# Kernel optimization log

Measured on AMD Instinct MI355X. Metric: run time of the kernel, lower is better.

Reference implementation:

```python
import jax, jax.numpy as jnp
import numpy as np

VOCAB = 1_000_000
EMBED = 128
N_DENSE = 13
N_SPARSE = 26
BATCH = 16384
BOT_DIMS = [512, 256, 128]
TOP_DIMS = [1024, 1024, 512, 256, 1]


def setup_inputs() -> dict:
    key = jax.random.key(0)
    ks = list(jax.random.split(key, 32))
    # input: 13 dense floats + 26 categorical ids (stored as floats, cast in fwd)
    dense = jax.random.normal(ks[0], (BATCH, N_DENSE), dtype=jnp.float32)
    cat = jax.random.randint(ks[1], (BATCH, N_SPARSE), 0, VOCAB).astype(jnp.float32)
    x = jnp.concatenate([dense, cat], axis=1)
    inp = {"x": x, "train": 0}
    # bottom MLP params
    fan_in = N_DENSE
    for i, d in enumerate(BOT_DIMS):
        s = (6.0 / (fan_in + d)) ** 0.5  # glorot uniform scale
        inp[f"bw{i}"] = jax.random.uniform(ks[2 + 2 * i], (fan_in, d), jnp.float32, -s, s)
        inp[f"bb{i}"] = jax.random.normal(ks[3 + 2 * i], (d,), jnp.float32) * (1.0 / d) ** 0.5
        fan_in = d
    # unified embedding table
    inp["emb"] = jax.random.uniform(ks[10], (VOCAB, EMBED), jnp.float32) / jnp.sqrt(float(VOCAB))
    # top MLP params; input dim = embed_dim + triu(27) = 128 + 378 = 506
    n_feat = 1 + N_SPARSE  # bottom output contributes one 128-dim feature row
    fan_in = EMBED + (n_feat * (n_feat + 1)) // 2
    for i, d in enumerate(TOP_DIMS):
        std = (2.0 / (fan_in + d)) ** 0.5
        inp[f"tw{i}"] = jax.random.normal(ks[12 + 2 * i], (fan_in, d), jnp.float32) * std
        inp[f"tb{i}"] = jax.random.normal(ks[13 + 2 * i], (d,), jnp.float32) * (1.0 / d) ** 0.5
        fan_in = d
    return inp


def dot_interact(f):
    # f: [B, n, d]; keep_diags=True -> upper-triangular (incl. diag) of f @ f^T
    n = f.shape[1]
    iu, ju = jnp.triu_indices(n)
    xact = jnp.einsum('bnd,bmd->bnm', f, f)  # [B, n, n]
    return xact[:, iu, ju]  # [B, n*(n+1)/2]


def reference(x, train, bw0, bb0, bw1, bb1, bw2, bb2, emb,
              tw0, tb0, tw1, tb1, tw2, tb2, tw3, tb3, tw4, tb4):
    del train
    dense, cat = jnp.split(x, [N_DENSE], axis=1)
    idx = jnp.reshape(cat.astype(jnp.int32), [-1]) % VOCAB
    # bottom MLP
    h = dense
    for w, b in ((bw0, bb0), (bw1, bb1), (bw2, bb2)):
        h = jax.nn.relu(h @ w + b)
    bot_out = h  # [B, 128]
    B = bot_out.shape[0]
    feat = jnp.reshape(bot_out, [B, -1, EMBED])  # [B, 1, 128]
    embf = jnp.reshape(emb[idx], [B, -1, EMBED])  # [B, 26, 128]
    feat = jnp.concatenate([feat, embf], axis=1)  # [B, 27, 128]
    inter = dot_interact(feat)  # [B, 378]
    t = jnp.concatenate([bot_out, inter], axis=-1)  # [B, 506]
    tops = [(tw0, tb0), (tw1, tb1), (tw2, tb2), (tw3, tb3), (tw4, tb4)]
    for i, (w, b) in enumerate(tops):
        t = t @ w + b
        if i < len(tops) - 1:
            t = jax.nn.relu(t)
    return t  # [B, 1] logits
```

## Files before the change

kernel.cpp:

```cpp
#include <hip/hip_runtime.h>

typedef float v4f  __attribute__((ext_vector_type(4)));
typedef __bf16 bf16x8 __attribute__((ext_vector_type(8)));

__device__ __forceinline__ unsigned short f2bf(float f) {
    unsigned u = __builtin_bit_cast(unsigned, f);
    u += 0x7FFFu + ((u >> 16) & 1u);
    return (unsigned short)(u >> 16);
}
__device__ __forceinline__ float bf2f(unsigned short h) {
    return __builtin_bit_cast(float, (unsigned)h << 16);
}

__device__ __forceinline__ void gload16(const unsigned short* g, unsigned short* l) {
    __builtin_amdgcn_global_load_lds(
        (const __attribute__((address_space(1))) unsigned int*)g,
        (__attribute__((address_space(3))) unsigned int*)l, 16, 0, 0);
}

#define M_BATCH 16384

__global__ __launch_bounds__(256) void wprep(const float* __restrict__ in,
                                             unsigned short* __restrict__ out,
                                             int K, int N, int Kpad) {
    __shared__ float tile[32][33];
    int tx = threadIdx.x & 31;
    int ty = threadIdx.x >> 5;
    int n0 = blockIdx.x * 32, k0 = blockIdx.y * 32;
#pragma unroll
    for (int i = 0; i < 32; i += 8) {
        int k = k0 + ty + i, n = n0 + tx;
        tile[ty + i][tx] = (k < K && n < N) ? in[(size_t)k * N + n] : 0.f;
    }
    __syncthreads();
#pragma unroll
    for (int i = 0; i < 32; i += 8) {
        int n = n0 + ty + i, k = k0 + tx;
        if (n < N && k < Kpad) out[(size_t)n * Kpad + k] = f2bf(tile[tx][ty + i]);
    }
}

__global__ __launch_bounds__(256) void bot0(const float* __restrict__ x,
                                            const float* __restrict__ w,
                                            const float* __restrict__ b,
                                            unsigned short* __restrict__ h0) {
    int gid = blockIdx.x * 256 + threadIdx.x;
    int row = gid >> 9, col = gid & 511;
    const float* xr = x + (size_t)row * 39;
    float acc = b[col];
#pragma unroll
    for (int k = 0; k < 13; k++) acc += xr[k] * w[k * 512 + col];
    h0[gid] = f2bf(fmaxf(acc, 0.f));
}

__global__ __launch_bounds__(256) void gemm_bt(const unsigned short* __restrict__ A,
                                               const unsigned short* __restrict__ Bt,
                                               const float* __restrict__ bias,
                                               unsigned short* __restrict__ C,
                                               int N, int K, int relu) {
    __shared__ __align__(16) unsigned short As0[128 * 32];
    __shared__ __align__(16) unsigned short Bs0[128 * 32];
    __shared__ __align__(16) unsigned short As1[128 * 32];
    __shared__ __align__(16) unsigned short Bs1[128 * 32];
    const int tid  = threadIdx.x;
    const int wave = tid >> 6, lane = tid & 63;
    const int quad = lane >> 4, r16 = lane & 15;
    const int m_blk = blockIdx.y * 128, n_blk = blockIdx.x * 128;
    const int w_m = (wave >> 1) * 64, w_n = (wave & 1) * 64;

    v4f acc[4][4] = {};

    const int slot0 = tid, slot1 = tid + 256;
    const int rowS0 = slot0 >> 2, chS0 = slot0 & 3;
    const int rowS1 = slot1 >> 2, chS1 = slot1 & 3;

    const unsigned short* pa0 = A  + (size_t)(m_blk + rowS0) * K + chS0 * 8;
    const unsigned short* pa1 = A  + (size_t)(m_blk + rowS1) * K + chS1 * 8;
    const unsigned short* pb0 = Bt + (size_t)(n_blk + rowS0) * K + chS0 * 8;
    const unsigned short* pb1 = Bt + (size_t)(n_blk + rowS1) * K + chS1 * 8;

#define STAGE(AsX, BsX, kk)                                   \
    do {                                                      \
        gload16(pa0 + (kk), AsX + slot0 * 8);                 \
        gload16(pa1 + (kk), AsX + slot1 * 8);                 \
        gload16(pb0 + (kk), BsX + slot0 * 8);                 \
        gload16(pb1 + (kk), BsX + slot1 * 8);                 \
    } while (0)

#define DRAIN_BAR()                                           \
    do {                                                      \
        asm volatile("s_waitcnt vmcnt(0)" ::: "memory");      \
        __builtin_amdgcn_s_barrier();                         \
        __builtin_amdgcn_sched_barrier(0);                    \
    } while (0)

#define COMPUTE(AsX, BsX)                                                         \
    do {                                                                          \
        bf16x8 af[4], bf[4];                                                      \
        _Pragma("unroll")                                                         \
        for (int i = 0; i < 4; i++)                                               \
            af[i] = *(const bf16x8*)(AsX + (w_m + i * 16 + r16) * 32 + quad * 8); \
        _Pragma("unroll")                                                         \
        for (int j = 0; j < 4; j++)                                               \
            bf[j] = *(const bf16x8*)(BsX + (w_n + j * 16 + r16) * 32 + quad * 8); \
        _Pragma("unroll")                                                         \
        for (int i = 0; i < 4; i++)                                               \
            _Pragma("unroll")                                                     \
            for (int j = 0; j < 4; j++)                                           \
                acc[i][j] = __builtin_amdgcn_mfma_f32_16x16x32_bf16(              \
                    af[i], bf[j], acc[i][j], 0, 0, 0);                            \
    } while (0)

    STAGE(As0, Bs0, 0);
    DRAIN_BAR();

    for (int k0 = 0; k0 < K; k0 += 64) {
        STAGE(As1, Bs1, k0 + 32);
        COMPUTE(As0, Bs0);
        DRAIN_BAR();
        if (k0 + 64 < K) STAGE(As0, Bs0, k0 + 64);
        COMPUTE(As1, Bs1);
        DRAIN_BAR();
    }
#undef STAGE
#undef DRAIN_BAR
#undef COMPUTE

#pragma unroll
    for (int j = 0; j < 4; j++) {
        int gcol = n_blk + w_n + j * 16 + r16;
        float bv = bias[gcol];
#pragma unroll
        for (int i = 0; i < 4; i++) {
            int grow = m_blk + w_m + i * 16 + quad * 4;
#pragma unroll
            for (int r = 0; r < 4; r++) {
                float v = acc[i][j][r] + bv;
                if (relu) v = fmaxf(v, 0.f);
                C[(size_t)(grow + r) * N + gcol] = f2bf(v);
            }
        }
    }
}

#define FS 136
__global__ __launch_bounds__(256) void interact(const float* __restrict__ x,
                                                const float* __restrict__ emb,
                                                const unsigned short* __restrict__ h2,
                                                unsigned short* __restrict__ top_in) {
    __shared__ __align__(16) unsigned short feat[4][32 * FS];
    __shared__ __align__(16) unsigned short rowb[4][512];
    const int wave = threadIdx.x >> 6, lane = threadIdx.x & 63;
    const int s = blockIdx.x * 4 + wave;
    unsigned short* fw = feat[wave];
    unsigned short* rb = rowb[wave];
    const int quad = lane >> 4, r16 = lane & 15;

    int cat = 0;
    if (lane < 26) cat = (int)x[(size_t)s * 39 + 13 + lane];
    if (lane < 16)
        *(uint4*)(fw + lane * 8) = *(const uint4*)(h2 + (size_t)s * 128 + lane * 8);
#pragma unroll
    for (int i = 0; i < 13; i++) {
        int t = i * 64 + lane;
        int row = t >> 5, c4 = t & 31;
        int id = __shfl(cat, row);
        float4 v = *(const float4*)(emb + (size_t)id * 128 + c4 * 4);
        ushort4 o;
        o.x = f2bf(v.x); o.y = f2bf(v.y); o.z = f2bf(v.z); o.w = f2bf(v.w);
        *(ushort4*)(fw + (size_t)(row + 1) * FS + c4 * 4) = o;
    }
    v4f c00 = {0,0,0,0}, c01 = {0,0,0,0}, c11 = {0,0,0,0};
#pragma unroll
    for (int kc = 0; kc < 4; kc++) {
        bf16x8 a0 = *(const bf16x8*)(fw + r16 * FS + kc * 32 + quad * 8);
        bf16x8 a1 = *(const bf16x8*)(fw + (16 + r16) * FS + kc * 32 + quad * 8);
        c00 = __builtin_amdgcn_mfma_f32_16x16x32_bf16(a0, a0, c00, 0, 0, 0);
        c01 = __builtin_amdgcn_mfma_f32_16x16x32_bf16(a0, a1, c01, 0, 0, 0);
        c11 = __builtin_amdgcn_mfma_f32_16x16x32_bf16(a1, a1, c11, 0, 0, 0);
    }
    if (lane < 16) *(uint4*)(rb + lane * 8) = *(const uint4*)(fw + lane * 8);
    if (lane < 6) rb[506 + lane] = 0;
#pragma unroll
    for (int r = 0; r < 4; r++) {
        int i = quad * 4 + r;
        int j = r16;
        if (i <= j)
            rb[128 + i * 27 - (i * (i - 1)) / 2 + (j - i)] = f2bf(c00[r]);
        int j2 = 16 + r16;
        if (j2 < 27) {
            rb[128 + i * 27 - (i * (i - 1)) / 2 + (j2 - i)] = f2bf(c01[r]);
            int ii = 16 + quad * 4 + r;
            if (ii <= j2)
                rb[128 + ii * 27 - (ii * (ii - 1)) / 2 + (j2 - ii)] = f2bf(c11[r]);
        }
    }
    *(uint4*)(top_in + (size_t)s * 512 + lane * 8) = *(const uint4*)(rb + lane * 8);
}

__global__ __launch_bounds__(256) void top_final(const unsigned short* __restrict__ ht3,
                                                 const float* __restrict__ w,
                                                 const float* __restrict__ b,
                                                 float* __restrict__ out) {
    int wave = threadIdx.x >> 6, lane = threadIdx.x & 63;
    int row = blockIdx.x * 4 + wave;
    ushort4 av = *(const ushort4*)(ht3 + (size_t)row * 256 + lane * 4);
    float4 wv = *(const float4*)(w + lane * 4);
    float s = bf2f(av.x) * wv.x + bf2f(av.y) * wv.y + bf2f(av.z) * wv.z + bf2f(av.w) * wv.w;
#pragma unroll
    for (int off = 32; off; off >>= 1) s += __shfl_down(s, off);
    if (lane == 0) out[row] = s + b[0];
}

extern "C" void kernel_launch(void* const* d_in, const int* in_sizes, int n_in,
                              void* d_out, int out_size, void* d_ws, size_t ws_size,
                              hipStream_t stream) {
    (void)in_sizes; (void)n_in; (void)out_size; (void)ws_size;
    const float* x   = (const float*)d_in[0];
    const float* bw0 = (const float*)d_in[2];
    const float* bb0 = (const float*)d_in[3];
    const float* bw1 = (const float*)d_in[4];
    const float* bb1 = (const float*)d_in[5];
    const float* bw2 = (const float*)d_in[6];
    const float* bb2 = (const float*)d_in[7];
    const float* emb = (const float*)d_in[8];
    const float* tw0 = (const float*)d_in[9];
    const float* tb0 = (const float*)d_in[10];
    const float* tw1 = (const float*)d_in[11];
    const float* tb1 = (const float*)d_in[12];
    const float* tw2 = (const float*)d_in[13];
    const float* tb2 = (const float*)d_in[14];
    const float* tw3 = (const float*)d_in[15];
    const float* tb3 = (const float*)d_in[16];
    const float* tw4 = (const float*)d_in[17];
    const float* tb4 = (const float*)d_in[18];
    float* out = (float*)d_out;

    char* ws = (char*)d_ws;
    size_t off = 0;
    auto alloc = [&](size_t bytes) {
        void* p = ws + off;
        off += (bytes + 255) & ~(size_t)255;
        return p;
    };
    unsigned short* bw1t = (unsigned short*)alloc((size_t)256 * 512 * 2);
    unsigned short* bw2t = (unsigned short*)alloc((size_t)128 * 256 * 2);
    unsigned short* tw0t = (unsigned short*)alloc((size_t)1024 * 512 * 2);
    unsigned short* tw1t = (unsigned short*)alloc((size_t)1024 * 1024 * 2);
    unsigned short* tw2t = (unsigned short*)alloc((size_t)512 * 1024 * 2);
    unsigned short* tw3t = (unsigned short*)alloc((size_t)256 * 512 * 2);
    unsigned short* h2   = (unsigned short*)alloc((size_t)M_BATCH * 128 * 2);
    unsigned short* bufA = (unsigned short*)alloc((size_t)M_BATCH * 1024 * 2);
    unsigned short* bufB = (unsigned short*)alloc((size_t)M_BATCH * 1024 * 2);

    unsigned short* h0     = bufA;
    unsigned short* h1     = bufB;
    unsigned short* top_in = bufA;
    unsigned short* ht0    = bufB;
    unsigned short* ht1    = bufA;
    unsigned short* ht2    = bufB;
    unsigned short* ht3    = bufA;

    dim3 blk(256);
    wprep<<<dim3(256 / 32,  512 / 32),  blk, 0, stream>>>(bw1,  bw1t, 512,  256,  512);
    wprep<<<dim3(128 / 32,  256 / 32),  blk, 0, stream>>>(bw2,  bw2t, 256,  128,  256);
    wprep<<<dim3(1024 / 32, 512 / 32),  blk, 0, stream>>>(tw0,  tw0t, 506,  1024, 512);
    wprep<<<dim3(1024 / 32, 1024 / 32), blk, 0, stream>>>(tw1,  tw1t, 1024, 1024, 1024);
    wprep<<<dim3(512 / 32,  1024 / 32), blk, 0, stream>>>(tw2,  tw2t, 1024, 512,  1024);
    wprep<<<dim3(256 / 32,  512 / 32),  blk, 0, stream>>>(tw3,  tw3t, 512,  256,  512);

    bot0<<<dim3(M_BATCH * 512 / 256), blk, 0, stream>>>(x, bw0, bb0, h0);
    gemm_bt<<<dim3(256 / 128, M_BATCH / 128), blk, 0, stream>>>(h0, bw1t, bb1, h1, 256, 512, 1);
    gemm_bt<<<dim3(128 / 128, M_BATCH / 128), blk, 0, stream>>>(h1, bw2t, bb2, h2, 128, 256, 1);

    interact<<<dim3(M_BATCH / 4), blk, 0, stream>>>(x, emb, h2, top_in);

    gemm_bt<<<dim3(1024 / 128, M_BATCH / 128), blk, 0, stream>>>(top_in, tw0t, tb0, ht0, 1024, 512, 1);
    gemm_bt<<<dim3(1024 / 128, M_BATCH / 128), blk, 0, stream>>>(ht0, tw1t, tb1, ht1, 1024, 1024, 1);
    gemm_bt<<<dim3(512 / 128,  M_BATCH / 128), blk, 0, stream>>>(ht1, tw2t, tb2, ht2, 512, 1024, 1);
    gemm_bt<<<dim3(256 / 128,  M_BATCH / 128), blk, 0, stream>>>(ht2, tw3t, tb3, ht3, 256, 512, 1);
    top_final<<<dim3(M_BATCH / 4), blk, 0, stream>>>(ht3, tw4, tb4, out);
}
```

Measured before the change: 847.3 us.

## Replace direct-to-LDS loads with register-staged prefetch and remap workgroups across XCDs

The GEMM main loop stops using global_load_lds with a full vmcnt(0) drain. It now prefetches two K-tiles ahead into registers, waits only with vmcnt(4), and writes to LDS before an lgkmcnt barrier, so global loads overlap the MFMA compute. It also remaps the workgroup index so consecutive logical tiles land on the same XCD, to improve L2 reuse. This costs more VGPRs for the staging registers and adds redundant loads of tile 0 on the last iterations.

```diff
diff --git a/kernel.cpp b/kernel.cpp
--- a/kernel.cpp
+++ b/kernel.cpp
@@ -10,12 +10,6 @@
 }
 __device__ __forceinline__ float bf2f(unsigned short h) {
     return __builtin_bit_cast(float, (unsigned)h << 16);
-}
-
-__device__ __forceinline__ void gload16(const unsigned short* g, unsigned short* l) {
-    __builtin_amdgcn_global_load_lds(
-        (const __attribute__((address_space(1))) unsigned int*)g,
-        (__attribute__((address_space(3))) unsigned int*)l, 16, 0, 0);
 }
 
 #define M_BATCH 16384
@@ -65,7 +59,15 @@
     const int tid  = threadIdx.x;
     const int wave = tid >> 6, lane = tid & 63;
     const int quad = lane >> 4, r16 = lane & 15;
-    const int m_blk = blockIdx.y * 128, n_blk = blockIdx.x * 128;
+
+    const int gx = gridDim.x;
+    const int nwg = gx * gridDim.y;
+    int d = blockIdx.y * gx + blockIdx.x;
+    int logical = d;
+    if ((nwg & 7) == 0) logical = (d & 7) * (nwg >> 3) + (d >> 3);
+    const int bx = logical % gx, by = logical / gx;
+
+    const int m_blk = by * 128, n_blk = bx * 128;
     const int w_m = (wave >> 1) * 64, w_n = (wave & 1) * 64;
 
     v4f acc[4][4] = {};
@@ -79,19 +81,22 @@
     const unsigned short* pb0 = Bt + (size_t)(n_blk + rowS0) * K + chS0 * 8;
     const unsigned short* pb1 = Bt + (size_t)(n_blk + rowS1) * K + chS1 * 8;
 
-#define STAGE(AsX, BsX, kk)                                   \
+    const int T = K >> 5;
+
+#define LOADSET(sA0, sA1, sB0, sB1, kk)                       \
     do {                                                      \
-        gload16(pa0 + (kk), AsX + slot0 * 8);                 \
-        gload16(pa1 + (kk), AsX + slot1 * 8);                 \
-        gload16(pb0 + (kk), BsX + slot0 * 8);                 \
-        gload16(pb1 + (kk), BsX + slot1 * 8);                 \
-    } while (0)
-
-#define DRAIN_BAR()                                           \
+        sA0 = *(const uint4*)(pa0 + (kk));                    \
+        sA1 = *(const uint4*)(pa1 + (kk));                    \
+        sB0 = *(const uint4*)(pb0 + (kk));                    \
+        sB1 = *(const uint4*)(pb1 + (kk));                    \
+    } while (0)
+
+#define WRITESET(AsX, BsX, sA0, sA1, sB0, sB1)                \
     do {                                                      \
-        asm volatile("s_waitcnt vmcnt(0)" ::: "memory");      \
-        __builtin_amdgcn_s_barrier();                         \
-        __builtin_amdgcn_sched_barrier(0);                    \
+        ((uint4*)AsX)[slot0] = sA0;                           \
+        ((uint4*)AsX)[slot1] = sA1;                           \
+        ((uint4*)BsX)[slot0] = sB0;                           \
+        ((uint4*)BsX)[slot1] = sB1;                           \
     } while (0)
 
 #define COMPUTE(AsX, BsX)                                                         \
@@ -111,20 +116,51 @@
                     af[i], bf[j], acc[i][j], 0, 0, 0);                            \
     } while (0)
 
-    STAGE(As0, Bs0, 0);
-    DRAIN_BAR();
-
-    for (int k0 = 0; k0 < K; k0 += 64) {
-        STAGE(As1, Bs1, k0 + 32);
-        COMPUTE(As0, Bs0);
-        DRAIN_BAR();
-        if (k0 + 64 < K) STAGE(As0, Bs0, k0 + 64);
-        COMPUTE(As1, Bs1);
-        DRAIN_BAR();
-    }
-#undef STAGE
-#undef DRAIN_BAR
+#define WAIT_VM4()                                            \
+    do {                                                      \
+        asm volatile("s_waitcnt vmcnt(4)" ::: "memory");      \
+        __builtin_amdgcn_sched_barrier(0);                    \
+    } while (0)
+
+#define LGKM0_BAR()                                           \
+    do {                                                      \
+        asm volatile("s_waitcnt lgkmcnt(0)" ::: "memory");    \
+        __builtin_amdgcn_sched_barrier(0);                    \
+        __builtin_amdgcn_s_barrier();                         \
+    } while (0)
+
+    uint4 aA0, aA1, aB0, aB1;
+    uint4 bA0, bA1, bB0, bB1;
+
+    LOADSET(aA0, aA1, aB0, aB1, 0);
+    LOADSET(bA0, bA1, bB0, bB1, 32);
+    WAIT_VM4();
+    WRITESET(As0, Bs0, aA0, aA1, aB0, aB1);
+    LGKM0_BAR();
+
+    for (int t = 0; t < T; t += 2) {
+        {
+            int kk = (t + 2 < T) ? (t + 2) * 32 : 0;
+            LOADSET(aA0, aA1, aB0, aB1, kk);
+            COMPUTE(As0, Bs0);
+            WAIT_VM4();
+            WRITESET(As1, Bs1, bA0, bA1, bB0, bB1);
+            LGKM0_BAR();
+        }
+        {
+            int kk = (t + 3 < T) ? (t + 3) * 32 : 0;
+            LOADSET(bA0, bA1, bB0, bB1, kk);
+            COMPUTE(As1, Bs1);
+            WAIT_VM4();
+            WRITESET(As0, Bs0, aA0, aA1, aB0, aB1);
+            LGKM0_BAR();
+        }
+    }
+#undef LOADSET
+#undef WRITESET
 #undef COMPUTE
+#undef WAIT_VM4
+#undef LGKM0_BAR
 
 #pragma unroll
     for (int j = 0; j < 4; j++) {
```

New measurement: 811.2 us. -4.3%, faster.
